# Kernel optimization log

Measured on AMD Instinct MI355X. Metric: run time of the kernel, lower is better.

The kernel has to match this reference:

```python
import jax, jax.numpy as jnp
import numpy as np

# Problem dims (see shape_source): batch, coils, simultaneous bands, grid, k-space pts
B, C, NB = 2, 8, 3
X, Y = 80, 80
M = 4096


def _to_c(a):
    # trailing dim 2 -> complex (old torch.fft convention)
    return a[..., 0] + 1j * a[..., 1]


def _to_r(z):
    return jnp.stack([jnp.real(z), jnp.imag(z)], axis=-1)


def setup_inputs() -> dict:
    key = jax.random.key(0)
    k1, k2, k3, k4 = jax.random.split(key, 4)
    x = jax.random.normal(k1, (B, NB, X, Y, 2), dtype=jnp.float32)
    maps = jax.random.normal(k2, (B, C, NB, X, Y, 2), dtype=jnp.float32) * 0.3
    phi = jax.random.normal(k3, (B, NB, M, 2), dtype=jnp.float32)
    # non-Cartesian k-space coordinates in sigpy convention: [-N/2, N/2)
    coord = (jax.random.uniform(k4, (B, M, 2), dtype=jnp.float32) - 0.5) * X
    return {"x": x, "maps": maps, "phi": phi, "coord": coord}


def _nudft_matrix(coord):
    # Exact (type-2) non-uniform DFT encoding matrix, [M, X*Y] complex64.
    # This is the operator the sigpy NUFFT (KB gridding) approximates.
    rx = jnp.arange(X, dtype=jnp.float32) - X // 2
    ry = jnp.arange(Y, dtype=jnp.float32) - Y // 2
    ph = (coord[:, 0, None, None] * rx[None, :, None] / X
          + coord[:, 1, None, None] * ry[None, None, :] / Y)  # [M, X, Y]
    E = jnp.exp((-2j * jnp.pi) * ph).astype(jnp.complex64)
    return E.reshape(M, X * Y) / np.float32(np.sqrt(X * Y))


def _forward_one(xc, mc, pc, coord):
    # A = S * P * F * C  (per batch item)
    E = _nudft_matrix(coord)                       # [M, XY]
    cimg = (mc * xc[None]).reshape(C, NB, X * Y)   # coil-sens multiply
    ksp = jnp.einsum('mp,cbp->cbm', E, cimg)       # NUFFT, [C, NB, M]
    return jnp.sum(pc[None] * ksp, axis=1)         # phase basis + band sum -> [C, M]


def reference(x, maps, phi, coord):
    xc, mc, pc = _to_c(x), _to_c(maps), _to_c(phi)
    out = jax.vmap(_forward_one)(xc, mc, pc, coord)  # [B, C, M] complex
    return _to_r(out)                                # [B, C, M, 2]
```

## Files before the change

kernel.cpp:

```cpp
#include <hip/hip_runtime.h>
#include <hip/hip_fp16.h>
#include <math.h>

#define B_   2
#define C_   8
#define NB_  3
#define X_   80
#define Y_   80
#define M_   4096
#define P_   6400
#define NJ   24
#define KS   3
#define NF   2
#define XS_  8
#define XPB_ (X_/XS_)
#define TWO_PI 6.2831853071795864769f

typedef _Float16 f16x8 __attribute__((ext_vector_type(8)));
typedef float    f32x4 __attribute__((ext_vector_type(4)));
typedef unsigned int u32x4 __attribute__((ext_vector_type(4)));

#define T1_ (B_*X_*KS*NF*64*8)
#define T2_ (B_*256*KS*512)

__device__ __forceinline__ int klocal(int lane, int i) {
  return ((lane >> 4) << 2) + (i & 3) + ((i >> 2) << 4);
}

__device__ __forceinline__ f16x8 negh8(f16x8 v) {
  u32x4 u = __builtin_bit_cast(u32x4, v);
  u ^= (u32x4){0x80008000u, 0x80008000u, 0x80008000u, 0x80008000u};
  return __builtin_bit_cast(f16x8, u);
}

__device__ __forceinline__ void sincos_rev(float t, float* s, float* c) {
  t -= rintf(t);
  __sincosf(-TWO_PI * t, s, c);
}

__global__ void prep_fused(const float* __restrict__ xin, const float* __restrict__ maps,
                           const float* __restrict__ coord,
                           _Float16* __restrict__ Bf,
                           _Float16* __restrict__ ARe, _Float16* __restrict__ AIm) {
  int t = blockIdx.x * blockDim.x + threadIdx.x;
  if (t < T1_) {
    int i    = t & 7;
    int lane = (t >> 3) & 63;
    int nf   = (t >> 9) & 1;
    int rest = t >> 10;
    int ks   = rest % 3; rest /= 3;
    int x    = rest % 80;
    int b    = rest / 80;

    int j = nf*16 + (lane & 15);
    int y = ks*32 + klocal(lane, i);
    float re = 0.f, im = 0.f;
    if (y < Y_ && j < NJ) {
      int c = j & 7, nb = j >> 3;
      int p = x*Y_ + y;
      const float* xp = xin  + (((size_t)b*NB_ + nb)*P_ + p)*2;
      const float* mp = maps + ((((size_t)b*C_ + c)*NB_ + nb)*P_ + p)*2;
      float xr = xp[0], xi2 = xp[1], mr = mp[0], mi = mp[1];
      re = mr*xr - mi*xi2;
      im = mr*xi2 + mi*xr;
    }
    size_t base = (size_t)((b*X_ + x)*6 + (ks*2 + nf)) * 1024;
    Bf[base + lane*8 + i]       = (_Float16)re;
    Bf[base + 512 + lane*8 + i] = (_Float16)im;
  } else {
    int u = t - T1_;
    int i    = u & 7;
    int lane = (u >> 3) & 63;
    int q    = u >> 9;
    int ks   = q % 3;
    int bm   = q / 3;
    int m16  = bm & 255;
    int b    = bm >> 8;

    int m = m16*16 + (lane & 15);
    int y = ks*32 + klocal(lane, i);
    float re = 0.f, im = 0.f;
    if (y < Y_) {
      float c1 = coord[((size_t)b*M_ + m)*2 + 1];
      float s, c;
      sincos_rev(c1 * (float)(y - 40) * (1.0f/80.0f), &s, &c);
      re = c * (1.0f/80.0f);
      im = s * (1.0f/80.0f);
    }
    ARe[u] = (_Float16)re;
    AIm[u] = (_Float16)im;
  }
}

__device__ __forceinline__ void stage_b(const _Float16* src, _Float16* dst, int tid) {
  int wave = tid >> 6, lane = tid & 63;
  #pragma unroll
  for (int u = 0; u < 3; u++) {
    int off = wave*3072 + u*1024;
    __builtin_amdgcn_global_load_lds(
      (const __attribute__((address_space(1))) void*)((const char*)src + off + lane*16),
      (__attribute__((address_space(3))) void*)((char*)dst + off),
      16, 0, 0);
  }
}

__global__ __launch_bounds__(256, 2) void main_mfma(
    const float* __restrict__ coord, const _Float16* __restrict__ Bf,
    const _Float16* __restrict__ ARe, const _Float16* __restrict__ AIm,
    const float* __restrict__ phi, float* __restrict__ partial) {
  __shared__ unsigned int extab[XPB_ * 128];
  __shared__ _Float16 bsm[2][6144];

  int mb   = blockIdx.x;
  int xs   = blockIdx.y;
  int b    = blockIdx.z;
  int tid  = threadIdx.x;
  int wave = tid >> 6, lane = tid & 63;
  int mblock = mb * 128;

  const _Float16* bfbase = Bf + (size_t)(b*X_ + xs*XPB_) * 6144;

  stage_b(bfbase, bsm[0], tid);

  for (int t = tid; t < XPB_*128; t += 256) {
    int xloc = t >> 7, ml = t & 127;
    int x = xs*XPB_ + xloc;
    float c0 = coord[((size_t)b*M_ + mblock + ml)*2 + 0];
    float s, c;
    sincos_rev(c0 * (float)(x - 40) * (1.0f/80.0f), &s, &c);
    __half2 h = __floats2half2_rn(c, s);
    extab[t] = *(unsigned int*)&h;
  }

  int mtile = mblock + wave*32;
  f16x8 ar[2][KS], ai[2][KS];
  #pragma unroll
  for (int mf = 0; mf < 2; mf++) {
    int m16 = (mtile >> 4) + mf;
    #pragma unroll
    for (int ks = 0; ks < KS; ks++) {
      size_t o = (((size_t)(b*256 + m16)*3 + ks)*512) + lane*8;
      ar[mf][ks] = *(const f16x8*)(ARe + o);
      ai[mf][ks] = *(const f16x8*)(AIm + o);
    }
  }
  __syncthreads();

  f32x4 outr[2][NF], outi[2][NF];
  #pragma unroll
  for (int mf = 0; mf < 2; mf++)
    #pragma unroll
    for (int nf = 0; nf < NF; nf++) {
      outr[mf][nf] = (f32x4){0.f,0.f,0.f,0.f};
      outi[mf][nf] = (f32x4){0.f,0.f,0.f,0.f};
    }

  int cur = 0;
  for (int xi = 0; xi < XPB_; xi++) {
    if (xi + 1 < XPB_)
      stage_b(bfbase + (size_t)(xi + 1) * 6144, bsm[cur ^ 1], tid);

    const _Float16* fb = bsm[cur];
    f16x8 br[KS][NF], bi[KS][NF];
    #pragma unroll
    for (int ks = 0; ks < KS; ks++)
      #pragma unroll
      for (int nf = 0; nf < NF; nf++) {
        const _Float16* p = fb + (ks*2 + nf)*1024 + lane*8;
        br[ks][nf] = *(const f16x8*)p;
        bi[ks][nf] = *(const f16x8*)(p + 512);
      }

    f32x4 Tr[2][NF], Ti[2][NF];
    #pragma unroll
    for (int mf = 0; mf < 2; mf++)
      #pragma unroll
      for (int nf = 0; nf < NF; nf++) {
        Tr[mf][nf] = (f32x4){0.f,0.f,0.f,0.f};
        Ti[mf][nf] = (f32x4){0.f,0.f,0.f,0.f};
      }

    #pragma unroll
    for (int ks = 0; ks < KS; ks++)
      #pragma unroll
      for (int mf = 0; mf < 2; mf++)
        #pragma unroll
        for (int nf = 0; nf < NF; nf++) {
          Tr[mf][nf] = __builtin_amdgcn_mfma_f32_16x16x32_f16(ar[mf][ks],        br[ks][nf], Tr[mf][nf], 0, 0, 0);
          Tr[mf][nf] = __builtin_amdgcn_mfma_f32_16x16x32_f16(negh8(ai[mf][ks]), bi[ks][nf], Tr[mf][nf], 0, 0, 0);
          Ti[mf][nf] = __builtin_amdgcn_mfma_f32_16x16x32_f16(ar[mf][ks],        bi[ks][nf], Ti[mf][nf], 0, 0, 0);
          Ti[mf][nf] = __builtin_amdgcn_mfma_f32_16x16x32_f16(ai[mf][ks],        br[ks][nf], Ti[mf][nf], 0, 0, 0);
        }

    #pragma unroll
    for (int mf = 0; mf < 2; mf++)
      #pragma unroll
      for (int r = 0; r < 4; r++) {
        int ml = wave*32 + mf*16 + ((lane >> 4) << 2) + r;
        unsigned int u = extab[xi*128 + ml];
        __half2 h = *(__half2*)&u;
        float exr = __low2float(h), exi = __high2float(h);
        #pragma unroll
        for (int nf = 0; nf < NF; nf++) {
          float tr = Tr[mf][nf][r], ti = Ti[mf][nf][r];
          outr[mf][nf][r] += exr*tr - exi*ti;
          outi[mf][nf][r] += exr*ti + exi*tr;
        }
      }

    __syncthreads();
    cur ^= 1;
  }

  int j0 = lane & 15;
  int row = (lane >> 4) << 2;
  const float* phb = phi + (size_t)b*NB_*M_*2;
  #pragma unroll
  for (int mf = 0; mf < 2; mf++)
    #pragma unroll
    for (int r = 0; r < 4; r++) {
      int m = mtile + mf*16 + row + r;
      const float* p0 = phb + ((size_t)(j0 >> 3)*M_ + m)*2;
      float p0r = p0[0], p0i = p0[1];
      float a0r = outr[mf][0][r], a0i = outi[mf][0][r];
      float vr = p0r*a0r - p0i*a0i;
      float vi = p0r*a0i + p0i*a0r;
      vr += __shfl_xor(vr, 8);
      vi += __shfl_xor(vi, 8);
      const float* p1 = phb + ((size_t)2*M_ + m)*2;
      float p1r = p1[0], p1i = p1[1];
      float a1r = outr[mf][1][r], a1i = outi[mf][1][r];
      vr += p1r*a1r - p1i*a1i;
      vi += p1r*a1i + p1i*a1r;
      if (j0 < 8) {
        int c = j0;
        size_t o = (((size_t)xs*B_ + b)*C_ + c)*M_ + m;
        ((float2*)partial)[o] = make_float2(vr, vi);
      }
    }
}

__global__ void combine3(const float* __restrict__ partial, float* __restrict__ out) {
  int t = blockIdx.x * blockDim.x + threadIdx.x;
  if (t >= B_*C_*M_) return;
  int m = t & (M_ - 1);
  int c = (t >> 12) & 7;
  int b = t >> 15;
  float sr = 0.f, si = 0.f;
  #pragma unroll
  for (int xs = 0; xs < XS_; xs++) {
    const float2 v = ((const float2*)partial)[(((size_t)xs*B_ + b)*C_ + c)*M_ + m];
    sr += v.x; si += v.y;
  }
  ((float2*)out)[((size_t)b*C_ + c)*M_ + m] = make_float2(sr, si);
}

extern "C" void kernel_launch(void* const* d_in, const int* in_sizes, int n_in,
                              void* d_out, int out_size, void* d_ws, size_t ws_size,
                              hipStream_t stream) {
  const float* xin   = (const float*)d_in[0];
  const float* maps  = (const float*)d_in[1];
  const float* phi   = (const float*)d_in[2];
  const float* coord = (const float*)d_in[3];
  float* out = (float*)d_out;

  const size_t bf_elems = (size_t)B_ * X_ * 6144;
  const size_t af_elems = (size_t)B_ * 256 * KS * 512;
  _Float16* Bf  = (_Float16*)d_ws;
  _Float16* ARe = Bf + bf_elems;
  _Float16* AIm = ARe + af_elems;
  float* partial = (float*)(AIm + af_elems);

  {
    int total = T1_ + T2_;
    prep_fused<<<(total + 255)/256, 256, 0, stream>>>(xin, maps, coord, Bf, ARe, AIm);
  }
  {
    dim3 g(M_/128, XS_, B_);
    main_mfma<<<g, 256, 0, stream>>>(coord, Bf, ARe, AIm, phi, partial);
  }
  {
    int total = B_*C_*M_;
    combine3<<<(total + 255)/256, 256, 0, stream>>>(partial, out);
  }
}
```

Measured before the change: 32.78 us.

## Use 3-mult complex GEMM and fuse partial reduction via last-block atomic counter

Replaces the four real MFMAs per complex product with three (Gauss/Karatsuba trick) by precomputing Are+Aim and Bre+Bim sums in fp16. It also removes the separate combine kernel: each block bumps an atomic counter, and the last of the x-slice blocks for a given m-block sums the partials and writes the output. Counters are zeroed in the prep kernel. The trick adds fp16 additions whose sums may lose precision or overflow range, and the atomic/threadfence handshake adds a serialized tail to one block.

```diff
diff --git a/kernel.cpp b/kernel.cpp
--- a/kernel.cpp
+++ b/kernel.cpp
@@ -27,12 +27,6 @@
   return ((lane >> 4) << 2) + (i & 3) + ((i >> 2) << 4);
 }
 
-__device__ __forceinline__ f16x8 negh8(f16x8 v) {
-  u32x4 u = __builtin_bit_cast(u32x4, v);
-  u ^= (u32x4){0x80008000u, 0x80008000u, 0x80008000u, 0x80008000u};
-  return __builtin_bit_cast(f16x8, u);
-}
-
 __device__ __forceinline__ void sincos_rev(float t, float* s, float* c) {
   t -= rintf(t);
   __sincosf(-TWO_PI * t, s, c);
@@ -41,7 +35,9 @@
 __global__ void prep_fused(const float* __restrict__ xin, const float* __restrict__ maps,
                            const float* __restrict__ coord,
                            _Float16* __restrict__ Bf,
-                           _Float16* __restrict__ ARe, _Float16* __restrict__ AIm) {
+                           _Float16* __restrict__ ARe, _Float16* __restrict__ AIm,
+                           int* __restrict__ cnt) {
+  if (blockIdx.x == 0 && threadIdx.x < 64) cnt[threadIdx.x] = 0;
   int t = blockIdx.x * blockDim.x + threadIdx.x;
   if (t < T1_) {
     int i    = t & 7;
@@ -107,9 +103,11 @@
 __global__ __launch_bounds__(256, 2) void main_mfma(
     const float* __restrict__ coord, const _Float16* __restrict__ Bf,
     const _Float16* __restrict__ ARe, const _Float16* __restrict__ AIm,
-    const float* __restrict__ phi, float* __restrict__ partial) {
+    const float* __restrict__ phi, float* __restrict__ partial,
+    float* __restrict__ out, int* __restrict__ cnt) {
   __shared__ unsigned int extab[XPB_ * 128];
   __shared__ _Float16 bsm[2][6144];
+  __shared__ int lastflag;
 
   int mb   = blockIdx.x;
   int xs   = blockIdx.y;
@@ -133,7 +131,7 @@
   }
 
   int mtile = mblock + wave*32;
-  f16x8 ar[2][KS], ai[2][KS];
+  f16x8 ar[2][KS], ai[2][KS], as_[2][KS];
   #pragma unroll
   for (int mf = 0; mf < 2; mf++) {
     int m16 = (mtile >> 4) + mf;
@@ -142,6 +140,7 @@
       size_t o = (((size_t)(b*256 + m16)*3 + ks)*512) + lane*8;
       ar[mf][ks] = *(const f16x8*)(ARe + o);
       ai[mf][ks] = *(const f16x8*)(AIm + o);
+      as_[mf][ks] = ar[mf][ks] + ai[mf][ks];
     }
   }
   __syncthreads();
@@ -161,7 +160,7 @@
       stage_b(bfbase + (size_t)(xi + 1) * 6144, bsm[cur ^ 1], tid);
 
     const _Float16* fb = bsm[cur];
-    f16x8 br[KS][NF], bi[KS][NF];
+    f16x8 br[KS][NF], bi[KS][NF], bs[KS][NF];
     #pragma unroll
     for (int ks = 0; ks < KS; ks++)
       #pragma unroll
@@ -169,15 +168,17 @@
         const _Float16* p = fb + (ks*2 + nf)*1024 + lane*8;
         br[ks][nf] = *(const f16x8*)p;
         bi[ks][nf] = *(const f16x8*)(p + 512);
-      }
-
-    f32x4 Tr[2][NF], Ti[2][NF];
+        bs[ks][nf] = br[ks][nf] + bi[ks][nf];
+      }
+
+    f32x4 M1[2][NF], M2[2][NF], M3[2][NF];
     #pragma unroll
     for (int mf = 0; mf < 2; mf++)
       #pragma unroll
       for (int nf = 0; nf < NF; nf++) {
-        Tr[mf][nf] = (f32x4){0.f,0.f,0.f,0.f};
-        Ti[mf][nf] = (f32x4){0.f,0.f,0.f,0.f};
+        M1[mf][nf] = (f32x4){0.f,0.f,0.f,0.f};
+        M2[mf][nf] = (f32x4){0.f,0.f,0.f,0.f};
+        M3[mf][nf] = (f32x4){0.f,0.f,0.f,0.f};
       }
 
     #pragma unroll
@@ -186,27 +187,28 @@
       for (int mf = 0; mf < 2; mf++)
         #pragma unroll
         for (int nf = 0; nf < NF; nf++) {
-          Tr[mf][nf] = __builtin_amdgcn_mfma_f32_16x16x32_f16(ar[mf][ks],        br[ks][nf], Tr[mf][nf], 0, 0, 0);
-          Tr[mf][nf] = __builtin_amdgcn_mfma_f32_16x16x32_f16(negh8(ai[mf][ks]), bi[ks][nf], Tr[mf][nf], 0, 0, 0);
-          Ti[mf][nf] = __builtin_amdgcn_mfma_f32_16x16x32_f16(ar[mf][ks],        bi[ks][nf], Ti[mf][nf], 0, 0, 0);
-          Ti[mf][nf] = __builtin_amdgcn_mfma_f32_16x16x32_f16(ai[mf][ks],        br[ks][nf], Ti[mf][nf], 0, 0, 0);
+          M1[mf][nf] = __builtin_amdgcn_mfma_f32_16x16x32_f16(ar[mf][ks],  br[ks][nf], M1[mf][nf], 0, 0, 0);
+          M2[mf][nf] = __builtin_amdgcn_mfma_f32_16x16x32_f16(ai[mf][ks],  bi[ks][nf], M2[mf][nf], 0, 0, 0);
+          M3[mf][nf] = __builtin_amdgcn_mfma_f32_16x16x32_f16(as_[mf][ks], bs[ks][nf], M3[mf][nf], 0, 0, 0);
         }
 
     #pragma unroll
-    for (int mf = 0; mf < 2; mf++)
-      #pragma unroll
-      for (int r = 0; r < 4; r++) {
-        int ml = wave*32 + mf*16 + ((lane >> 4) << 2) + r;
-        unsigned int u = extab[xi*128 + ml];
-        __half2 h = *(__half2*)&u;
-        float exr = __low2float(h), exi = __high2float(h);
+    for (int mf = 0; mf < 2; mf++) {
+      #pragma unroll
+      for (int nf = 0; nf < NF; nf++) {
+        f32x4 tr = M1[mf][nf] - M2[mf][nf];
+        f32x4 ti = M3[mf][nf] - M1[mf][nf] - M2[mf][nf];
         #pragma unroll
-        for (int nf = 0; nf < NF; nf++) {
-          float tr = Tr[mf][nf][r], ti = Ti[mf][nf][r];
-          outr[mf][nf][r] += exr*tr - exi*ti;
-          outi[mf][nf][r] += exr*ti + exi*tr;
+        for (int r = 0; r < 4; r++) {
+          int ml = wave*32 + mf*16 + ((lane >> 4) << 2) + r;
+          unsigned int u = extab[xi*128 + ml];
+          __half2 h = *(__half2*)&u;
+          float exr = __low2float(h), exi = __high2float(h);
+          outr[mf][nf][r] += exr*tr[r] - exi*ti[r];
+          outi[mf][nf][r] += exr*ti[r] + exi*tr[r];
         }
       }
+    }
 
     __syncthreads();
     cur ^= 1;
@@ -238,21 +240,28 @@
         ((float2*)partial)[o] = make_float2(vr, vi);
       }
     }
-}
-
-__global__ void combine3(const float* __restrict__ partial, float* __restrict__ out) {
-  int t = blockIdx.x * blockDim.x + threadIdx.x;
-  if (t >= B_*C_*M_) return;
-  int m = t & (M_ - 1);
-  int c = (t >> 12) & 7;
-  int b = t >> 15;
-  float sr = 0.f, si = 0.f;
-  #pragma unroll
-  for (int xs = 0; xs < XS_; xs++) {
-    const float2 v = ((const float2*)partial)[(((size_t)xs*B_ + b)*C_ + c)*M_ + m];
-    sr += v.x; si += v.y;
-  }
-  ((float2*)out)[((size_t)b*C_ + c)*M_ + m] = make_float2(sr, si);
+
+  __threadfence();
+  __syncthreads();
+  if (tid == 0) {
+    int old = atomicAdd(&cnt[b*32 + mb], 1);
+    lastflag = (old == XS_ - 1);
+  }
+  __syncthreads();
+  if (lastflag) {
+    __threadfence();
+    for (int t = tid; t < C_*128; t += 256) {
+      int c = t >> 7, mloc = t & 127;
+      int m = mblock + mloc;
+      float sr = 0.f, si = 0.f;
+      #pragma unroll
+      for (int x2 = 0; x2 < XS_; x2++) {
+        const float2 v = ((const float2*)partial)[(((size_t)x2*B_ + b)*C_ + c)*M_ + m];
+        sr += v.x; si += v.y;
+      }
+      ((float2*)out)[((size_t)b*C_ + c)*M_ + m] = make_float2(sr, si);
+    }
+  }
 }
 
 extern "C" void kernel_launch(void* const* d_in, const int* in_sizes, int n_in,
@@ -270,17 +279,14 @@
   _Float16* ARe = Bf + bf_elems;
   _Float16* AIm = ARe + af_elems;
   float* partial = (float*)(AIm + af_elems);
+  int* cnt = (int*)(partial + (size_t)XS_*B_*C_*M_*2);
 
   {
     int total = T1_ + T2_;
-    prep_fused<<<(total + 255)/256, 256, 0, stream>>>(xin, maps, coord, Bf, ARe, AIm);
+    prep_fused<<<(total + 255)/256, 256, 0, stream>>>(xin, maps, coord, Bf, ARe, AIm, cnt);
   }
   {
     dim3 g(M_/128, XS_, B_);
-    main_mfma<<<g, 256, 0, stream>>>(coord, Bf, ARe, AIm, phi, partial);
-  }
-  {
-    int total = B_*C_*M_;
-    combine3<<<(total + 255)/256, 256, 0, stream>>>(partial, out);
-  }
-}
+    main_mfma<<<g, 256, 0, stream>>>(coord, Bf, ARe, AIm, phi, partial, out, cnt);
+  }
+}
```

Result: slower. 96.45 us (+194.2%).
